# Optimization experiments

Measured on AMD Instinct MI355X. Metric: run time of the kernel, lower is better.

The kernel has to match this reference:

```python
import jax, jax.numpy as jnp
import numpy as np

HIDDEN = 64
SLOTS = 4
SEQ = 24
VOCAB = 64
B = 16384


def setup_inputs() -> dict:
    key = jax.random.key(0)
    ks = jax.random.split(key, 12)
    def w(k, shape):
        return (jax.random.normal(k, shape, jnp.float32) * 0.05).astype(jnp.float32)
    return {
        "seqs": jax.random.randint(ks[0], (B, SEQ), 0, VOCAB + 2),
        "query_tok": jax.random.randint(ks[1], (B,), 0, VOCAB + 2),
        "embed": w(ks[2], (VOCAB + 2, HIDDEN)),
        "wg_w1": w(ks[3], (HIDDEN, 32)), "wg_b1": jnp.zeros((32,), jnp.float32),
        "wg_w2": w(ks[4], (32, 1)),      "wg_b2": jnp.zeros((1,), jnp.float32),
        "eg_w1": w(ks[5], (2 * HIDDEN, 32)), "eg_b1": jnp.zeros((32,), jnp.float32),
        "eg_w2": w(ks[6], (32, 1)),          "eg_b2": jnp.zeros((1,), jnp.float32),
        "rh_w1": w(ks[7], (2 * HIDDEN, HIDDEN)), "rh_b1": jnp.zeros((HIDDEN,), jnp.float32),
        "rh_w2": w(ks[8], (HIDDEN, VOCAB)),      "rh_b2": jnp.zeros((VOCAB,), jnp.float32),
    }


def reference(seqs, query_tok, embed,
              wg_w1, wg_b1, wg_w2, wg_b2,
              eg_w1, eg_b1, eg_w2, eg_b2,
              rh_w1, rh_b1, rh_w2, rh_b2):
    Bsz = seqs.shape[0]
    toks = seqs[:, :SEQ - 1].T  # [T-1, B], scanned over time

    def step(mem, tok):
        # mem: [B, SLOTS, HIDDEN]
        ne = embed[tok]  # [B, HIDDEN]
        # write gate: sigmoid scalar per token
        w = jax.nn.sigmoid(jnp.maximum(ne @ wg_w1 + wg_b1, 0.0) @ wg_w2 + wg_b2)  # [B,1]
        # evict gate on cat(new_emb, mem[s]) for every slot, vectorized
        ei = jnp.concatenate(
            [jnp.broadcast_to(ne[:, None, :], (Bsz, SLOTS, HIDDEN)), mem], axis=-1)  # [B,S,2H]
        el = (jnp.maximum(ei @ eg_w1 + eg_b1, 0.0) @ eg_w2 + eg_b2)[..., 0]  # [B,S]
        oh = jax.nn.one_hot(jnp.argmax(el, axis=-1), SLOTS, dtype=mem.dtype)  # [B,S]
        newv = (ne * w)[:, None, :]  # [B,1,H]
        mem = mem * (1.0 - oh[..., None]) + oh[..., None] * newv
        return mem, None

    mem0 = jnp.zeros((Bsz, SLOTS, HIDDEN), embed.dtype)
    mem, _ = jax.lax.scan(step, mem0, toks)

    q = embed[query_tok]                              # [B,H]
    r = jnp.concatenate([q, mem.mean(axis=1)], -1)    # [B,2H]
    logits = jnp.maximum(r @ rh_w1 + rh_b1, 0.0) @ rh_w2 + rh_b2  # [B,VOCAB]
    return logits
```

## Files before the change

### kernel.cpp

```cpp
#include <hip/hip_runtime.h>
#include <math.h>

#define SEQT 24
#define NSTEP 23
#define NTOK 66
#define NSLOT_ST 67

__global__ __launch_bounds__(256) void k_tables(
    const float* __restrict__ embed,
    const float* __restrict__ wg_w1, const float* __restrict__ wg_b1,
    const float* __restrict__ wg_w2, const float* __restrict__ wg_b2,
    const float* __restrict__ eg_w1, const float* __restrict__ eg_b1,
    const float* __restrict__ rh_w1, const float* __restrict__ rh_b1,
    double* __restrict__ t_u,
    double* __restrict__ t_vnwT,
    float*  __restrict__ t_qh1,
    float*  __restrict__ t_ebw)
{
    const int a = blockIdx.x;
    const int t = threadIdx.x;
    __shared__ float  s_e[64];
    __shared__ double s_h[32];
    __shared__ double s_w;

    if (t < 64) s_e[t] = embed[a * 64 + t];
    __syncthreads();

    const float* wp = nullptr;
    int stride = 32, col = 0;
    if      (t < 32)  { wp = eg_w1;            col = t;       }
    else if (t < 64)  { wp = eg_w1 + 64 * 32;  col = t - 32;  }
    else if (t < 96)  { wp = wg_w1;            col = t - 64;  }
    else if (t < 160) { wp = rh_w1;            col = t - 96;  stride = 64; }
    else if (t < 224) { wp = rh_w1 + 64 * 64;  col = t - 160; stride = 64; }

    double acc = 0.0;
    if (t < 224) {
        #pragma unroll 8
        for (int k = 0; k < 64; ++k)
            acc += (double)s_e[k] * (double)wp[k * stride + col];
    }

    if (t >= 64 && t < 96) {
        const int j = t - 64;
        double hr = acc + (double)wg_b1[j];
        if (hr < 0.0) hr = 0.0;
        s_h[j] = hr * (double)wg_w2[j];
    }
    __syncthreads();
    if (t == 0) {
        double z = (double)wg_b2[0];
        for (int j = 0; j < 32; ++j) z += s_h[j];
        s_w = 1.0 / (1.0 + exp(-z));
    }
    __syncthreads();
    const double w = s_w;

    if      (t < 32)  { t_u[a * 32 + t] = acc + (double)eg_b1[t];
                        if (a == 0) t_vnwT[t * NSLOT_ST + 66] = 0.0; }
    else if (t < 64)  { t_vnwT[col * NSLOT_ST + a] = w * acc; }
    else if (t >= 96 && t < 160) { t_qh1[a * 64 + col] = (float)(acc + (double)rh_b1[col]); }
    else if (t >= 160 && t < 224) { t_ebw[a * 64 + col] = (float)(0.25 * w * acc); }
}

__global__ __launch_bounds__(256) void k_el(
    const double* __restrict__ t_u, const double* __restrict__ t_vnwT,
    const float* __restrict__ eg_w2, const float* __restrict__ eg_b2,
    float* __restrict__ t_EL)
{
    const int tid = blockIdx.x * 256 + threadIdx.x;
    if (tid >= NTOK * NSLOT_ST) return;
    const int a = tid / NSLOT_ST;
    const int b = tid - a * NSLOT_ST;
    double acc = (double)eg_b2[0];
    #pragma unroll
    for (int j = 0; j < 32; ++j) {
        const double v = t_u[a * 32 + j] + t_vnwT[j * NSLOT_ST + b];
        if (v > 0.0) acc += v * (double)eg_w2[j];
    }
    t_EL[tid] = (float)acc;
}

__global__ __launch_bounds__(256) void k_main(
    const int* __restrict__ seqs, const int* __restrict__ query_tok,
    const float* __restrict__ t_EL, const float* __restrict__ t_qh1,
    const float* __restrict__ t_ebw,
    const float* __restrict__ rh_w2, const float* __restrict__ rh_b2,
    float* __restrict__ out)
{
    __shared__ __align__(16) float sEL[NTOK * NSLOT_ST];
    __shared__ __align__(16) float s_qh1[NTOK * 64];
    __shared__ __align__(16) float s_ebw[NSLOT_ST * 64];
    __shared__ int s_state[64];

    const int tid = threadIdx.x;

    for (int i = tid; i < NTOK * NSLOT_ST; i += 256) sEL[i] = t_EL[i];
    __syncthreads();

    const int wv = tid >> 6, lane = tid & 63;

    if (wv == 0) {
        const int b = blockIdx.x * 64 + lane;
        const int4* rp = (const int4*)(seqs + b * SEQT);
        const int4 q0 = rp[0], q1 = rp[1], q2 = rp[2], q3 = rp[3], q4 = rp[4], q5 = rp[5];
        int row[24];
        row[0]=q0.x;  row[1]=q0.y;  row[2]=q0.z;  row[3]=q0.w;
        row[4]=q1.x;  row[5]=q1.y;  row[6]=q1.z;  row[7]=q1.w;
        row[8]=q2.x;  row[9]=q2.y;  row[10]=q2.z; row[11]=q2.w;
        row[12]=q3.x; row[13]=q3.y; row[14]=q3.z; row[15]=q3.w;
        row[16]=q4.x; row[17]=q4.y; row[18]=q4.z; row[19]=q4.w;
        row[20]=q5.x; row[21]=q5.y; row[22]=q5.z; row[23]=q5.w;

        int ts0 = 66, ts1 = 66, ts2 = 66, ts3 = 66;
        #pragma unroll
        for (int t = 0; t < NSTEP; ++t) {
            const int tok  = row[t];
            const int base = tok * NSLOT_ST;
            const float e0 = sEL[base + ts0];
            const float e1 = sEL[base + ts1];
            const float e2 = sEL[base + ts2];
            const float e3 = sEL[base + ts3];
            int bi = 0; float best = e0;
            if (e1 > best) { best = e1; bi = 1; }
            if (e2 > best) { best = e2; bi = 2; }
            if (e3 > best) { best = e3; bi = 3; }
            ts0 = (bi == 0) ? tok : ts0;
            ts1 = (bi == 1) ? tok : ts1;
            ts2 = (bi == 2) ? tok : ts2;
            ts3 = (bi == 3) ? tok : ts3;
        }
        s_state[lane] = ts0 | (ts1 << 8) | (ts2 << 16) | (ts3 << 24);
    } else {
        const float4* gq = (const float4*)t_qh1;
        const float4* ge = (const float4*)t_ebw;
        float4* sq = (float4*)s_qh1;
        float4* se = (float4*)s_ebw;
        for (int i = tid - 64; i < 2112; i += 192) {
            if (i < 1056) sq[i] = gq[i];
            else          se[i - 1056] = ge[i - 1056];
        }
        if (tid < 128) s_ebw[NTOK * 64 + (tid - 64)] = 0.0f;
    }
    __syncthreads();

    float w2c[64];
    #pragma unroll
    for (int k = 0; k < 64; ++k) w2c[k] = rh_w2[k * 64 + lane];
    const float rb2 = rh_b2[lane];

    for (int i = 0; i < 16; ++i) {
        const int e  = wv * 16 + i;
        const int bg = blockIdx.x * 64 + e;
        const int qt = query_tok[bg];
        const unsigned st = (unsigned)s_state[e];
        const int u0 = st & 255, u1 = (st >> 8) & 255,
                  u2 = (st >> 16) & 255, u3 = st >> 24;
        float h1 = s_qh1[qt * 64 + lane]
                 + s_ebw[u0 * 64 + lane] + s_ebw[u1 * 64 + lane]
                 + s_ebw[u2 * 64 + lane] + s_ebw[u3 * 64 + lane];
        h1 = fmaxf(h1, 0.0f);

        float a0 = rb2, a1 = 0.0f, a2 = 0.0f, a3 = 0.0f;
        #pragma unroll
        for (int k = 0; k < 64; k += 4) {
            const float h0 = __uint_as_float(__builtin_amdgcn_readlane(__float_as_uint(h1), k));
            const float hA = __uint_as_float(__builtin_amdgcn_readlane(__float_as_uint(h1), k + 1));
            const float hB = __uint_as_float(__builtin_amdgcn_readlane(__float_as_uint(h1), k + 2));
            const float hC = __uint_as_float(__builtin_amdgcn_readlane(__float_as_uint(h1), k + 3));
            a0 = fmaf(h0, w2c[k],     a0);
            a1 = fmaf(hA, w2c[k + 1], a1);
            a2 = fmaf(hB, w2c[k + 2], a2);
            a3 = fmaf(hC, w2c[k + 3], a3);
        }
        out[bg * 64 + lane] = (a0 + a1) + (a2 + a3);
    }
}

extern "C" void kernel_launch(void* const* d_in, const int* in_sizes, int n_in,
                              void* d_out, int out_size, void* d_ws, size_t ws_size,
                              hipStream_t stream)
{
    const int*   seqs      = (const int*)  d_in[0];
    const int*   query_tok = (const int*)  d_in[1];
    const float* embed     = (const float*)d_in[2];
    const float* wg_w1     = (const float*)d_in[3];
    const float* wg_b1     = (const float*)d_in[4];
    const float* wg_w2     = (const float*)d_in[5];
    const float* wg_b2     = (const float*)d_in[6];
    const float* eg_w1     = (const float*)d_in[7];
    const float* eg_b1     = (const float*)d_in[8];
    const float* eg_w2     = (const float*)d_in[9];
    const float* eg_b2     = (const float*)d_in[10];
    const float* rh_w1     = (const float*)d_in[11];
    const float* rh_b1     = (const float*)d_in[12];
    const float* rh_w2     = (const float*)d_in[13];
    const float* rh_b2     = (const float*)d_in[14];
    float* out = (float*)d_out;
    const int B = in_sizes[1];

    double* t_u    = (double*)d_ws;
    double* t_vnwT = t_u + NTOK * 32;
    float*  t_qh1  = (float*)(t_vnwT + 32 * NSLOT_ST);
    float*  t_ebw  = t_qh1 + NTOK * 64;
    float*  t_EL   = t_ebw + NTOK * 64;

    k_tables<<<NTOK, 256, 0, stream>>>(embed, wg_w1, wg_b1, wg_w2, wg_b2,
                                       eg_w1, eg_b1, rh_w1, rh_b1,
                                       t_u, t_vnwT, t_qh1, t_ebw);
    k_el<<<(NTOK * NSLOT_ST + 255) / 256, 256, 0, stream>>>(t_u, t_vnwT, eg_w2, eg_b2, t_EL);
    k_main<<<B / 64, 256, 0, stream>>>(seqs, query_tok, t_EL, t_qh1, t_ebw,
                                       rh_w2, rh_b2, out);
}
```

Baseline: 33.61 us.

## Fuse table, evict-logit and main kernels into one cooperative kernel

Replaces the three launches with a single cooperative launch. The first 66 blocks build the per-token tables, then a grid-wide sync follows. Every block then recomputes the full evict-logit table in shared memory from padded LDS copies of the intermediate tables, instead of relying on a separate small kernel. This removes two kernel launches and the global round trip of the logit table. In exchange, each block repeats the fp64 logit-table work and pays for a grid barrier.

```diff
diff --git a/kernel.cpp b/kernel.cpp
--- a/kernel.cpp
+++ b/kernel.cpp
@@ -1,102 +1,110 @@
 #include <hip/hip_runtime.h>
+#include <hip/hip_cooperative_groups.h>
 #include <math.h>
+
+namespace cg = cooperative_groups;
 
 #define SEQT 24
 #define NSTEP 23
 #define NTOK 66
-#define NSLOT_ST 67
-
-__global__ __launch_bounds__(256) void k_tables(
+#define NST 67
+
+__global__ __launch_bounds__(256) void k_coop(
+    const int* __restrict__ seqs, const int* __restrict__ query_tok,
     const float* __restrict__ embed,
     const float* __restrict__ wg_w1, const float* __restrict__ wg_b1,
     const float* __restrict__ wg_w2, const float* __restrict__ wg_b2,
     const float* __restrict__ eg_w1, const float* __restrict__ eg_b1,
+    const float* __restrict__ eg_w2, const float* __restrict__ eg_b2,
     const float* __restrict__ rh_w1, const float* __restrict__ rh_b1,
+    const float* __restrict__ rh_w2, const float* __restrict__ rh_b2,
+    float* __restrict__ out,
     double* __restrict__ t_u,
     double* __restrict__ t_vnwT,
     float*  __restrict__ t_qh1,
     float*  __restrict__ t_ebw)
 {
-    const int a = blockIdx.x;
-    const int t = threadIdx.x;
-    __shared__ float  s_e[64];
-    __shared__ double s_h[32];
-    __shared__ double s_w;
-
-    if (t < 64) s_e[t] = embed[a * 64 + t];
+    __shared__ __align__(16) double sA[2178];
+    __shared__ __align__(16) double sB[2176];
+    __shared__ __align__(16) float  sEL[NTOK * NST];
+    __shared__ int s_state[64];
+
+    const int tid = threadIdx.x;
+    cg::grid_group grid = cg::this_grid();
+
+    if (blockIdx.x < NTOK) {
+        double* s_h = (double*)sEL;
+        float*  s_e = (float*)(sEL + 128);
+        double* s_wp = (double*)(sEL + 300);
+
+        const int a = blockIdx.x;
+        const int t = tid;
+        if (t < 64) s_e[t] = embed[a * 64 + t];
+        __syncthreads();
+
+        const float* wp = nullptr;
+        int stride = 32, col = 0;
+        if      (t < 32)  { wp = eg_w1;            col = t;       }
+        else if (t < 64)  { wp = eg_w1 + 64 * 32;  col = t - 32;  }
+        else if (t < 96)  { wp = wg_w1;            col = t - 64;  }
+        else if (t < 160) { wp = rh_w1;            col = t - 96;  stride = 64; }
+        else if (t < 224) { wp = rh_w1 + 64 * 64;  col = t - 160; stride = 64; }
+
+        double acc = 0.0;
+        if (t < 224) {
+            #pragma unroll 8
+            for (int k = 0; k < 64; ++k)
+                acc += (double)s_e[k] * (double)wp[k * stride + col];
+        }
+
+        if (t >= 64 && t < 96) {
+            const int j = t - 64;
+            double hr = acc + (double)wg_b1[j];
+            if (hr < 0.0) hr = 0.0;
+            s_h[j] = hr * (double)wg_w2[j];
+        }
+        __syncthreads();
+        if (t == 0) {
+            double z = (double)wg_b2[0];
+            for (int j = 0; j < 32; ++j) z += s_h[j];
+            s_wp[0] = 1.0 / (1.0 + exp(-z));
+        }
+        __syncthreads();
+        const double w = s_wp[0];
+
+        if      (t < 32)  { t_u[a * 32 + t] = acc + (double)eg_b1[t];
+                            if (a == 0) t_vnwT[t * NST + 66] = 0.0; }
+        else if (t < 64)  { t_vnwT[col * NST + a] = w * acc; }
+        else if (t >= 96 && t < 160)  { t_qh1[a * 64 + col] = (float)(acc + (double)rh_b1[col]); }
+        else if (t >= 160 && t < 224) { t_ebw[a * 64 + col] = (float)(0.25 * w * acc); }
+        __threadfence();
+    }
+
+    grid.sync();
+
+    for (int i = tid; i < NTOK * 32; i += 256)
+        sA[(i >> 5) * 33 + (i & 31)] = t_u[i];
+    for (int i = tid; i < 32 * NST; i += 256) {
+        const int j = i / NST, b = i - j * NST;
+        sB[j * 68 + b] = t_vnwT[i];
+    }
     __syncthreads();
 
-    const float* wp = nullptr;
-    int stride = 32, col = 0;
-    if      (t < 32)  { wp = eg_w1;            col = t;       }
-    else if (t < 64)  { wp = eg_w1 + 64 * 32;  col = t - 32;  }
-    else if (t < 96)  { wp = wg_w1;            col = t - 64;  }
-    else if (t < 160) { wp = rh_w1;            col = t - 96;  stride = 64; }
-    else if (t < 224) { wp = rh_w1 + 64 * 64;  col = t - 160; stride = 64; }
-
-    double acc = 0.0;
-    if (t < 224) {
-        #pragma unroll 8
-        for (int k = 0; k < 64; ++k)
-            acc += (double)s_e[k] * (double)wp[k * stride + col];
-    }
-
-    if (t >= 64 && t < 96) {
-        const int j = t - 64;
-        double hr = acc + (double)wg_b1[j];
-        if (hr < 0.0) hr = 0.0;
-        s_h[j] = hr * (double)wg_w2[j];
+    const double eb2 = (double)eg_b2[0];
+    for (int it = tid; it < NTOK * NST; it += 256) {
+        const int a = it / NST, b = it - a * NST;
+        double acc = eb2;
+        #pragma unroll
+        for (int j = 0; j < 32; ++j) {
+            const double v = sA[a * 33 + j] + sB[j * 68 + b];
+            if (v > 0.0) acc += v * (double)eg_w2[j];
+        }
+        sEL[it] = (float)acc;
     }
     __syncthreads();
-    if (t == 0) {
-        double z = (double)wg_b2[0];
-        for (int j = 0; j < 32; ++j) z += s_h[j];
-        s_w = 1.0 / (1.0 + exp(-z));
-    }
-    __syncthreads();
-    const double w = s_w;
-
-    if      (t < 32)  { t_u[a * 32 + t] = acc + (double)eg_b1[t];
-                        if (a == 0) t_vnwT[t * NSLOT_ST + 66] = 0.0; }
-    else if (t < 64)  { t_vnwT[col * NSLOT_ST + a] = w * acc; }
-    else if (t >= 96 && t < 160) { t_qh1[a * 64 + col] = (float)(acc + (double)rh_b1[col]); }
-    else if (t >= 160 && t < 224) { t_ebw[a * 64 + col] = (float)(0.25 * w * acc); }
-}
-
-__global__ __launch_bounds__(256) void k_el(
-    const double* __restrict__ t_u, const double* __restrict__ t_vnwT,
-    const float* __restrict__ eg_w2, const float* __restrict__ eg_b2,
-    float* __restrict__ t_EL)
-{
-    const int tid = blockIdx.x * 256 + threadIdx.x;
-    if (tid >= NTOK * NSLOT_ST) return;
-    const int a = tid / NSLOT_ST;
-    const int b = tid - a * NSLOT_ST;
-    double acc = (double)eg_b2[0];
-    #pragma unroll
-    for (int j = 0; j < 32; ++j) {
-        const double v = t_u[a * 32 + j] + t_vnwT[j * NSLOT_ST + b];
-        if (v > 0.0) acc += v * (double)eg_w2[j];
-    }
-    t_EL[tid] = (float)acc;
-}
-
-__global__ __launch_bounds__(256) void k_main(
-    const int* __restrict__ seqs, const int* __restrict__ query_tok,
-    const float* __restrict__ t_EL, const float* __restrict__ t_qh1,
-    const float* __restrict__ t_ebw,
-    const float* __restrict__ rh_w2, const float* __restrict__ rh_b2,
-    float* __restrict__ out)
-{
-    __shared__ __align__(16) float sEL[NTOK * NSLOT_ST];
-    __shared__ __align__(16) float s_qh1[NTOK * 64];
-    __shared__ __align__(16) float s_ebw[NSLOT_ST * 64];
-    __shared__ int s_state[64];
-
-    const int tid = threadIdx.x;
-
-    for (int i = tid; i < NTOK * NSLOT_ST; i += 256) sEL[i] = t_EL[i];
-    __syncthreads();
+
+    float* s_qh1 = (float*)sA;
+    float* s_ebw = (float*)sB;
 
     const int wv = tid >> 6, lane = tid & 63;
 
@@ -116,7 +124,7 @@
         #pragma unroll
         for (int t = 0; t < NSTEP; ++t) {
             const int tok  = row[t];
-            const int base = tok * NSLOT_ST;
+            const int base = tok * NST;
             const float e0 = sEL[base + ts0];
             const float e1 = sEL[base + ts1];
             const float e2 = sEL[base + ts2];
@@ -201,14 +209,16 @@
 
     double* t_u    = (double*)d_ws;
     double* t_vnwT = t_u + NTOK * 32;
-    float*  t_qh1  = (float*)(t_vnwT + 32 * NSLOT_ST);
+    float*  t_qh1  = (float*)(t_vnwT + 32 * NST);
     float*  t_ebw  = t_qh1 + NTOK * 64;
-    float*  t_EL   = t_ebw + NTOK * 64;
-
-    k_tables<<<NTOK, 256, 0, stream>>>(embed, wg_w1, wg_b1, wg_w2, wg_b2,
-                                       eg_w1, eg_b1, rh_w1, rh_b1,
-                                       t_u, t_vnwT, t_qh1, t_ebw);
-    k_el<<<(NTOK * NSLOT_ST + 255) / 256, 256, 0, stream>>>(t_u, t_vnwT, eg_w2, eg_b2, t_EL);
-    k_main<<<B / 64, 256, 0, stream>>>(seqs, query_tok, t_EL, t_qh1, t_ebw,
-                                       rh_w2, rh_b2, out);
+
+    void* kargs[] = {
+        (void*)&seqs, (void*)&query_tok, (void*)&embed,
+        (void*)&wg_w1, (void*)&wg_b1, (void*)&wg_w2, (void*)&wg_b2,
+        (void*)&eg_w1, (void*)&eg_b1, (void*)&eg_w2, (void*)&eg_b2,
+        (void*)&rh_w1, (void*)&rh_b1, (void*)&rh_w2, (void*)&rh_b2,
+        (void*)&out, (void*)&t_u, (void*)&t_vnwT, (void*)&t_qh1, (void*)&t_ebw
+    };
+    hipLaunchCooperativeKernel((void*)k_coop, dim3(B / 64), dim3(256),
+                               kargs, 0, stream);
 }
```

After: 104.5 us. 3.11x slower.

## Fuse table and evict-logit kernels, halve batch rows per main block

Applied to the files above, without the earlier changes.

Merges the two precompute kernels into one 11-block kernel. Each block redundantly computes the per-token u table in shared memory and then produces its slice of the evict-logit table, which removes one launch and its global round trip. The main kernel now handles 32 batch rows per block instead of 64, which doubles the grid. It also issues the sequence loads before the EL table copy and vectorizes that copy. In exchange, each main block reloads the shared tables for fewer rows, and the table kernel duplicates the u-table work across blocks.

```diff
diff --git a/kernel.cpp b/kernel.cpp
--- a/kernel.cpp
+++ b/kernel.cpp
@@ -4,81 +4,113 @@
 #define SEQT 24
 #define NSTEP 23
 #define NTOK 66
-#define NSLOT_ST 67
+#define NST 67
+#define NB 32
 
 __global__ __launch_bounds__(256) void k_tables(
     const float* __restrict__ embed,
     const float* __restrict__ wg_w1, const float* __restrict__ wg_b1,
     const float* __restrict__ wg_w2, const float* __restrict__ wg_b2,
     const float* __restrict__ eg_w1, const float* __restrict__ eg_b1,
+    const float* __restrict__ eg_w2, const float* __restrict__ eg_b2,
     const float* __restrict__ rh_w1, const float* __restrict__ rh_b1,
-    double* __restrict__ t_u,
-    double* __restrict__ t_vnwT,
-    float*  __restrict__ t_qh1,
-    float*  __restrict__ t_ebw)
+    float* __restrict__ t_EL,
+    float* __restrict__ t_qh1,
+    float* __restrict__ t_ebw)
 {
-    const int a = blockIdx.x;
-    const int t = threadIdx.x;
-    __shared__ float  s_e[64];
-    __shared__ double s_h[32];
-    __shared__ double s_w;
-
-    if (t < 64) s_e[t] = embed[a * 64 + t];
-    __syncthreads();
-
-    const float* wp = nullptr;
-    int stride = 32, col = 0;
-    if      (t < 32)  { wp = eg_w1;            col = t;       }
-    else if (t < 64)  { wp = eg_w1 + 64 * 32;  col = t - 32;  }
-    else if (t < 96)  { wp = wg_w1;            col = t - 64;  }
-    else if (t < 160) { wp = rh_w1;            col = t - 96;  stride = 64; }
-    else if (t < 224) { wp = rh_w1 + 64 * 64;  col = t - 160; stride = 64; }
-
-    double acc = 0.0;
-    if (t < 224) {
+    __shared__ __align__(16) float s_emb[NTOK * 64];
+    __shared__ double s_u[NTOK][33];
+    __shared__ double s_nb[6][33];
+    __shared__ double s_h[6][33];
+    __shared__ double s_wnb[7][33];
+    __shared__ double s_qraw[6 * 64];
+    __shared__ double s_ebraw[6 * 64];
+    __shared__ double s_w[6];
+
+    const int tid = threadIdx.x;
+    const int blk = blockIdx.x;
+    const int b0  = blk * 6;
+
+    {
+        const float4* ge = (const float4*)embed;
+        float4* se = (float4*)s_emb;
+        for (int i = tid; i < 1056; i += 256) se[i] = ge[i];
+    }
+    __syncthreads();
+
+    for (int base = 0; base < 3264; base += 1024) {
+        const float* wp[4]; int st[4], col[4], er[4], dd[4]; bool act[4];
+        #pragma unroll
+        for (int m = 0; m < 4; ++m) {
+            int d = base + tid + m * 256;
+            act[m] = d < 3264; dd[m] = d;
+            int dc = act[m] ? d : 0;
+            if (dc < 2112)      { wp[m] = eg_w1;           st[m] = 32; col[m] = dc & 31; er[m] = dc >> 5; }
+            else if (dc < 2304) { int x = dc - 2112; wp[m] = eg_w1 + 64 * 32; st[m] = 32; col[m] = x & 31; er[m] = b0 + (x >> 5); }
+            else if (dc < 2496) { int x = dc - 2304; wp[m] = wg_w1;           st[m] = 32; col[m] = x & 31; er[m] = b0 + (x >> 5); }
+            else if (dc < 2880) { int x = dc - 2496; wp[m] = rh_w1;           st[m] = 64; col[m] = x & 63; er[m] = b0 + (x >> 6); }
+            else                { int x = dc - 2880; wp[m] = rh_w1 + 64 * 64; st[m] = 64; col[m] = x & 63; er[m] = b0 + (x >> 6); }
+        }
+        double acc[4] = {0.0, 0.0, 0.0, 0.0};
         #pragma unroll 8
-        for (int k = 0; k < 64; ++k)
-            acc += (double)s_e[k] * (double)wp[k * stride + col];
-    }
-
-    if (t >= 64 && t < 96) {
-        const int j = t - 64;
-        double hr = acc + (double)wg_b1[j];
-        if (hr < 0.0) hr = 0.0;
-        s_h[j] = hr * (double)wg_w2[j];
-    }
-    __syncthreads();
-    if (t == 0) {
+        for (int k = 0; k < 64; ++k) {
+            #pragma unroll
+            for (int m = 0; m < 4; ++m)
+                acc[m] += (double)s_emb[er[m] * 64 + k] * (double)wp[m][k * st[m] + col[m]];
+        }
+        #pragma unroll
+        for (int m = 0; m < 4; ++m) {
+            if (!act[m]) continue;
+            const int d = dd[m];
+            if (d < 2112) {
+                s_u[d >> 5][d & 31] = acc[m] + (double)eg_b1[d & 31];
+            } else if (d < 2304) {
+                const int x = d - 2112; s_nb[x >> 5][x & 31] = acc[m];
+            } else if (d < 2496) {
+                const int x = d - 2304, j = x & 31;
+                double hr = acc[m] + (double)wg_b1[j];
+                if (hr < 0.0) hr = 0.0;
+                s_h[x >> 5][j] = hr * (double)wg_w2[j];
+            } else if (d < 2880) {
+                s_qraw[d - 2496] = acc[m];
+            } else {
+                s_ebraw[d - 2880] = acc[m];
+            }
+        }
+    }
+    __syncthreads();
+
+    if (tid < 6) {
         double z = (double)wg_b2[0];
-        for (int j = 0; j < 32; ++j) z += s_h[j];
-        s_w = 1.0 / (1.0 + exp(-z));
-    }
-    __syncthreads();
-    const double w = s_w;
-
-    if      (t < 32)  { t_u[a * 32 + t] = acc + (double)eg_b1[t];
-                        if (a == 0) t_vnwT[t * NSLOT_ST + 66] = 0.0; }
-    else if (t < 64)  { t_vnwT[col * NSLOT_ST + a] = w * acc; }
-    else if (t >= 96 && t < 160) { t_qh1[a * 64 + col] = (float)(acc + (double)rh_b1[col]); }
-    else if (t >= 160 && t < 224) { t_ebw[a * 64 + col] = (float)(0.25 * w * acc); }
-}
-
-__global__ __launch_bounds__(256) void k_el(
-    const double* __restrict__ t_u, const double* __restrict__ t_vnwT,
-    const float* __restrict__ eg_w2, const float* __restrict__ eg_b2,
-    float* __restrict__ t_EL)
-{
-    const int tid = blockIdx.x * 256 + threadIdx.x;
-    if (tid >= NTOK * NSLOT_ST) return;
-    const int a = tid / NSLOT_ST;
-    const int b = tid - a * NSLOT_ST;
-    double acc = (double)eg_b2[0];
-    #pragma unroll
-    for (int j = 0; j < 32; ++j) {
-        const double v = t_u[a * 32 + j] + t_vnwT[j * NSLOT_ST + b];
-        if (v > 0.0) acc += v * (double)eg_w2[j];
-    }
-    t_EL[tid] = (float)acc;
+        #pragma unroll
+        for (int j = 0; j < 32; ++j) z += s_h[tid][j];
+        s_w[tid] = 1.0 / (1.0 + exp(-z));
+    }
+    __syncthreads();
+
+    if (tid < 224) {
+        const int r = tid >> 5, j = tid & 31;
+        s_wnb[r][j] = (r < 6) ? s_w[r] * s_nb[r][j] : 0.0;
+    }
+    for (int x = tid; x < 384; x += 256) {
+        const int r = x >> 6, c = x & 63;
+        t_qh1[(b0 + r) * 64 + c] = (float)(s_qraw[x] + (double)rh_b1[c]);
+        t_ebw[(b0 + r) * 64 + c] = (float)(0.25 * s_w[r] * s_ebraw[x]);
+    }
+    __syncthreads();
+
+    const int ncol = (blk == 10) ? 7 : 6;
+    const double eb2 = (double)eg_b2[0];
+    for (int it = tid; it < NTOK * ncol; it += 256) {
+        const int a = it / ncol, r = it - a * ncol;
+        double acc = eb2;
+        #pragma unroll
+        for (int j = 0; j < 32; ++j) {
+            const double v = s_u[a][j] + s_wnb[r][j];
+            if (v > 0.0) acc += v * (double)eg_w2[j];
+        }
+        t_EL[a * NST + (b0 + r)] = (float)acc;
+    }
 }
 
 __global__ __launch_bounds__(256) void k_main(
@@ -88,49 +120,58 @@
     const float* __restrict__ rh_w2, const float* __restrict__ rh_b2,
     float* __restrict__ out)
 {
-    __shared__ __align__(16) float sEL[NTOK * NSLOT_ST];
+    __shared__ __align__(16) float sEL[NTOK * NST];
     __shared__ __align__(16) float s_qh1[NTOK * 64];
-    __shared__ __align__(16) float s_ebw[NSLOT_ST * 64];
-    __shared__ int s_state[64];
+    __shared__ __align__(16) float s_ebw[NST * 64];
+    __shared__ int s_state[NB];
 
     const int tid = threadIdx.x;
-
-    for (int i = tid; i < NTOK * NSLOT_ST; i += 256) sEL[i] = t_EL[i];
-    __syncthreads();
-
     const int wv = tid >> 6, lane = tid & 63;
 
+    int4 q0, q1, q2, q3, q4, q5;
+    if (wv == 0 && lane < NB) {
+        const int4* rp = (const int4*)(seqs + (blockIdx.x * NB + lane) * SEQT);
+        q0 = rp[0]; q1 = rp[1]; q2 = rp[2]; q3 = rp[3]; q4 = rp[4]; q5 = rp[5];
+    }
+
+    {
+        const float4* g4 = (const float4*)t_EL;
+        float4* s4 = (float4*)sEL;
+        for (int i = tid; i < 1105; i += 256) s4[i] = g4[i];
+        if (tid < 2) sEL[4420 + tid] = t_EL[4420 + tid];
+    }
+    __syncthreads();
+
     if (wv == 0) {
-        const int b = blockIdx.x * 64 + lane;
-        const int4* rp = (const int4*)(seqs + b * SEQT);
-        const int4 q0 = rp[0], q1 = rp[1], q2 = rp[2], q3 = rp[3], q4 = rp[4], q5 = rp[5];
-        int row[24];
-        row[0]=q0.x;  row[1]=q0.y;  row[2]=q0.z;  row[3]=q0.w;
-        row[4]=q1.x;  row[5]=q1.y;  row[6]=q1.z;  row[7]=q1.w;
-        row[8]=q2.x;  row[9]=q2.y;  row[10]=q2.z; row[11]=q2.w;
-        row[12]=q3.x; row[13]=q3.y; row[14]=q3.z; row[15]=q3.w;
-        row[16]=q4.x; row[17]=q4.y; row[18]=q4.z; row[19]=q4.w;
-        row[20]=q5.x; row[21]=q5.y; row[22]=q5.z; row[23]=q5.w;
-
-        int ts0 = 66, ts1 = 66, ts2 = 66, ts3 = 66;
-        #pragma unroll
-        for (int t = 0; t < NSTEP; ++t) {
-            const int tok  = row[t];
-            const int base = tok * NSLOT_ST;
-            const float e0 = sEL[base + ts0];
-            const float e1 = sEL[base + ts1];
-            const float e2 = sEL[base + ts2];
-            const float e3 = sEL[base + ts3];
-            int bi = 0; float best = e0;
-            if (e1 > best) { best = e1; bi = 1; }
-            if (e2 > best) { best = e2; bi = 2; }
-            if (e3 > best) { best = e3; bi = 3; }
-            ts0 = (bi == 0) ? tok : ts0;
-            ts1 = (bi == 1) ? tok : ts1;
-            ts2 = (bi == 2) ? tok : ts2;
-            ts3 = (bi == 3) ? tok : ts3;
-        }
-        s_state[lane] = ts0 | (ts1 << 8) | (ts2 << 16) | (ts3 << 24);
+        if (lane < NB) {
+            int row[24];
+            row[0]=q0.x;  row[1]=q0.y;  row[2]=q0.z;  row[3]=q0.w;
+            row[4]=q1.x;  row[5]=q1.y;  row[6]=q1.z;  row[7]=q1.w;
+            row[8]=q2.x;  row[9]=q2.y;  row[10]=q2.z; row[11]=q2.w;
+            row[12]=q3.x; row[13]=q3.y; row[14]=q3.z; row[15]=q3.w;
+            row[16]=q4.x; row[17]=q4.y; row[18]=q4.z; row[19]=q4.w;
+            row[20]=q5.x; row[21]=q5.y; row[22]=q5.z; row[23]=q5.w;
+
+            int ts0 = 66, ts1 = 66, ts2 = 66, ts3 = 66;
+            #pragma unroll
+            for (int t = 0; t < NSTEP; ++t) {
+                const int tok  = row[t];
+                const int base = tok * NST;
+                const float e0 = sEL[base + ts0];
+                const float e1 = sEL[base + ts1];
+                const float e2 = sEL[base + ts2];
+                const float e3 = sEL[base + ts3];
+                int bi = 0; float best = e0;
+                if (e1 > best) { best = e1; bi = 1; }
+                if (e2 > best) { best = e2; bi = 2; }
+                if (e3 > best) { best = e3; bi = 3; }
+                ts0 = (bi == 0) ? tok : ts0;
+                ts1 = (bi == 1) ? tok : ts1;
+                ts2 = (bi == 2) ? tok : ts2;
+                ts3 = (bi == 3) ? tok : ts3;
+            }
+            s_state[lane] = ts0 | (ts1 << 8) | (ts2 << 16) | (ts3 << 24);
+        }
     } else {
         const float4* gq = (const float4*)t_qh1;
         const float4* ge = (const float4*)t_ebw;
@@ -149,9 +190,9 @@
     for (int k = 0; k < 64; ++k) w2c[k] = rh_w2[k * 64 + lane];
     const float rb2 = rh_b2[lane];
 
-    for (int i = 0; i < 16; ++i) {
-        const int e  = wv * 16 + i;
-        const int bg = blockIdx.x * 64 + e;
+    for (int i = 0; i < 8; ++i) {
+        const int e  = wv * 8 + i;
+        const int bg = blockIdx.x * NB + e;
         const int qt = query_tok[bg];
         const unsigned st = (unsigned)s_state[e];
         const int u0 = st & 255, u1 = (st >> 8) & 255,
@@ -199,16 +240,13 @@
     float* out = (float*)d_out;
     const int B = in_sizes[1];
 
-    double* t_u    = (double*)d_ws;
-    double* t_vnwT = t_u + NTOK * 32;
-    float*  t_qh1  = (float*)(t_vnwT + 32 * NSLOT_ST);
-    float*  t_ebw  = t_qh1 + NTOK * 64;
-    float*  t_EL   = t_ebw + NTOK * 64;
-
-    k_tables<<<NTOK, 256, 0, stream>>>(embed, wg_w1, wg_b1, wg_w2, wg_b2,
-                                       eg_w1, eg_b1, rh_w1, rh_b1,
-                                       t_u, t_vnwT, t_qh1, t_ebw);
-    k_el<<<(NTOK * NSLOT_ST + 255) / 256, 256, 0, stream>>>(t_u, t_vnwT, eg_w2, eg_b2, t_EL);
-    k_main<<<B / 64, 256, 0, stream>>>(seqs, query_tok, t_EL, t_qh1, t_ebw,
+    float* t_EL  = (float*)d_ws;
+    float* t_qh1 = t_EL + 4432;
+    float* t_ebw = t_qh1 + 4224;
+
+    k_tables<<<11, 256, 0, stream>>>(embed, wg_w1, wg_b1, wg_w2, wg_b2,
+                                     eg_w1, eg_b1, eg_w2, eg_b2,
+                                     rh_w1, rh_b1, t_EL, t_qh1, t_ebw);
+    k_main<<<B / NB, 256, 0, stream>>>(seqs, query_tok, t_EL, t_qh1, t_ebw,
                                        rh_w2, rh_b2, out);
 }
```

New measurement: 38.73 us. 1.15x slower.
